# Optimization experiments

Hardware: AMD Instinct MI355X
Metric: run time of the kernel (lower is better)

The kernel has to match this reference:

```python
import jax, jax.numpy as jnp
import numpy as np

N = 100_000   # nodes
R = 8         # relations (edge types)
E = 100_000   # edges per relation
D_IN = 64
D_OUT = 64


def setup_inputs() -> dict:
    key = jax.random.key(0)
    k1, k2, k3, k4 = jax.random.split(key, 4)
    feat = jax.random.normal(k1, (N, D_IN), dtype=jnp.float32)
    # per-relation weight matrices (nn.ParameterDict in the original)
    weight = jax.random.normal(k2, (R, D_IN, D_OUT), dtype=jnp.float32) / np.sqrt(D_IN).astype(np.float32)
    edge_src = jax.random.randint(k3, (R, E), 0, N)
    edge_dst = jax.random.randint(k4, (R, E), 0, N)
    return {"feat": feat, "weight": weight, "edge_src": edge_src, "edge_dst": edge_dst}


def reference(feat, weight, edge_src, edge_dst):
    # Per-relation: gather src features, dense matmul with that relation's
    # weight, scatter-sum messages into destination nodes; 'sum' across
    # relations (cross-type reducer) collapses into one big scatter-add.
    n = feat.shape[0]
    gathered = feat[edge_src]                            # [R, E, d_in] irregular gather
    msg = jnp.einsum('red,rdf->ref', gathered, weight)   # [R, E, d_out]
    out = jax.ops.segment_sum(
        msg.reshape(-1, msg.shape[-1]),                  # [R*E, d_out]
        edge_dst.reshape(-1),
        num_segments=n,
    )                                                    # [N, d_out]
    return out
```

## Files before the change

### kernel.cpp

```cpp
#include <hip/hip_runtime.h>
#include <hip/hip_bf16.h>


#define WAVES_PER_BLOCK 4
#define EDGES_PER_WAVE 64
#define NGROUPS (EDGES_PER_WAVE / 4)
#define TILE_E (WAVES_PER_BLOCK * EDGES_PER_WAVE)

__global__ __launch_bounds__(256) void rgcn_edge_kernel(
    const float* __restrict__ feat,
    const float* __restrict__ weight,
    const int*   __restrict__ esrc,
    const int*   __restrict__ edst,
    float*       __restrict__ out,
    int E, int blocksPerRel)
{
    __shared__ float slab[WAVES_PER_BLOCK][4][64];

    const int t    = threadIdx.x;
    const int wave = t >> 6;
    const int lane = t & 63;

    const int r       = blockIdx.x / blocksPerRel;
    const int tileIdx = blockIdx.x % blocksPerRel;
    const int e0      = tileIdx * TILE_E + wave * EDGES_PER_WAVE;

    const float* wbase = weight + (size_t)r * 4096 + lane;
    float wreg[64];
    #pragma unroll
    for (int d = 0; d < 64; ++d) wreg[d] = wbase[(size_t)d * 64];

    const int sub = lane >> 4;
    const int q   = lane & 15;

    const int* srcR = esrc + (size_t)r * E;
    const int* dstR = edst + (size_t)r * E;

    auto load_group = [&](int gbase, float4& a, int dv[4]) {
        const int  e_g  = gbase + sub;
        const int  srow = (e_g < E) ? srcR[e_g] : 0;
        a = ((const float4*)(feat + (size_t)srow * 64))[q];
        if (gbase + 3 < E) {
            const int4 d4 = *(const int4*)(dstR + gbase);
            dv[0] = d4.x; dv[1] = d4.y; dv[2] = d4.z; dv[3] = d4.w;
        } else {
            #pragma unroll
            for (int s = 0; s < 4; ++s)
                dv[s] = (gbase + s < E) ? dstR[gbase + s] : 0;
        }
    };

    if (e0 >= E) return;

    float4 aCur; int dCur[4];
    load_group(e0, aCur, dCur);

    for (int g = 0; g < NGROUPS; ++g) {
        const int ebase = e0 + g * 4;
        if (ebase >= E) break;

        *(float4*)&slab[wave][sub][q * 4] = aCur;

        float4 aNxt = {0.f, 0.f, 0.f, 0.f};
        int dNxt[4] = {0, 0, 0, 0};
        const int enext = ebase + 4;
        const bool hasNext = (g + 1 < NGROUPS) && (enext < E);
        if (hasNext) load_group(enext, aNxt, dNxt);

        #pragma unroll
        for (int s = 0; s < 4; ++s) {
            const int e = ebase + s;
            if (e >= E) break;
            float acc = 0.f;
            #pragma unroll
            for (int d4 = 0; d4 < 16; ++d4) {
                const float4 av = *(const float4*)&slab[wave][s][d4 * 4];
                acc = fmaf(av.x, wreg[4 * d4 + 0], acc);
                acc = fmaf(av.y, wreg[4 * d4 + 1], acc);
                acc = fmaf(av.z, wreg[4 * d4 + 2], acc);
                acc = fmaf(av.w, wreg[4 * d4 + 3], acc);
            }
            atomicAdd(out + (size_t)dCur[s] * 64 + lane, acc);
        }

        aCur = aNxt;
        #pragma unroll
        for (int s = 0; s < 4; ++s) dCur[s] = dNxt[s];
    }
}

extern "C" void kernel_launch(void* const* d_in, const int* in_sizes, int n_in,
                              void* d_out, int out_size, void* d_ws, size_t ws_size,
                              hipStream_t stream) {
    const float* feat   = (const float*)d_in[0];
    const float* weight = (const float*)d_in[1];
    const int*   esrc   = (const int*)d_in[2];
    const int*   edst   = (const int*)d_in[3];
    float*       out    = (float*)d_out;

    const int R = in_sizes[1] / (64 * 64);
    const int E = in_sizes[2] / R;

    hipMemsetAsync(d_out, 0, (size_t)out_size * sizeof(float), stream);

    const int blocksPerRel = (E + TILE_E - 1) / TILE_E;
    const dim3 grid(R * blocksPerRel);
    const dim3 block(WAVES_PER_BLOCK * 64);
    rgcn_edge_kernel<<<grid, block, 0, stream>>>(feat, weight, esrc, edst, out,
                                                 E, blocksPerRel);
}
```

Baseline: 267.3 us.

## Broadcast edge indices via readlane and load source rows uniformly, dropping LDS staging

```diff
diff --git a/kernel.cpp b/kernel.cpp
--- a/kernel.cpp
+++ b/kernel.cpp
@@ -4,7 +4,6 @@
 
 #define WAVES_PER_BLOCK 4
 #define EDGES_PER_WAVE 64
-#define NGROUPS (EDGES_PER_WAVE / 4)
 #define TILE_E (WAVES_PER_BLOCK * EDGES_PER_WAVE)
 
 __global__ __launch_bounds__(256) void rgcn_edge_kernel(
@@ -15,8 +14,6 @@
     float*       __restrict__ out,
     int E, int blocksPerRel)
 {
-    __shared__ float slab[WAVES_PER_BLOCK][4][64];
-
     const int t    = threadIdx.x;
     const int wave = t >> 6;
     const int lane = t & 63;
@@ -24,68 +21,37 @@
     const int r       = blockIdx.x / blocksPerRel;
     const int tileIdx = blockIdx.x % blocksPerRel;
     const int e0      = tileIdx * TILE_E + wave * EDGES_PER_WAVE;
+    if (e0 >= E) return;
 
     const float* wbase = weight + (size_t)r * 4096 + lane;
     float wreg[64];
     #pragma unroll
     for (int d = 0; d < 64; ++d) wreg[d] = wbase[(size_t)d * 64];
 
-    const int sub = lane >> 4;
-    const int q   = lane & 15;
+    const int nE = min(EDGES_PER_WAVE, E - e0);
+    const int ei = e0 + min(lane, nE - 1);
+    const int sv = esrc[(size_t)r * E + ei];
+    const int dv = edst[(size_t)r * E + ei];
 
-    const int* srcR = esrc + (size_t)r * E;
-    const int* dstR = edst + (size_t)r * E;
+    float* outl = out + lane;
 
-    auto load_group = [&](int gbase, float4& a, int dv[4]) {
-        const int  e_g  = gbase + sub;
-        const int  srow = (e_g < E) ? srcR[e_g] : 0;
-        a = ((const float4*)(feat + (size_t)srow * 64))[q];
-        if (gbase + 3 < E) {
-            const int4 d4 = *(const int4*)(dstR + gbase);
-            dv[0] = d4.x; dv[1] = d4.y; dv[2] = d4.z; dv[3] = d4.w;
-        } else {
-            #pragma unroll
-            for (int s = 0; s < 4; ++s)
-                dv[s] = (gbase + s < E) ? dstR[gbase + s] : 0;
+    for (int i = 0; i < nE; ++i) {
+        const int srow = __builtin_amdgcn_readlane(sv, i);
+        const int drow = __builtin_amdgcn_readlane(dv, i);
+
+        const float4* xp = (const float4*)(feat + (size_t)srow * 64);
+        float a0 = 0.f, a1 = 0.f, a2 = 0.f, a3 = 0.f;
+        #pragma unroll
+        for (int c = 0; c < 16; ++c) {
+            const float4 v = xp[c];
+            a0 = fmaf(v.x, wreg[4 * c + 0], a0);
+            a1 = fmaf(v.y, wreg[4 * c + 1], a1);
+            a2 = fmaf(v.z, wreg[4 * c + 2], a2);
+            a3 = fmaf(v.w, wreg[4 * c + 3], a3);
         }
-    };
+        const float acc = (a0 + a1) + (a2 + a3);
 
-    if (e0 >= E) return;
-
-    float4 aCur; int dCur[4];
-    load_group(e0, aCur, dCur);
-
-    for (int g = 0; g < NGROUPS; ++g) {
-        const int ebase = e0 + g * 4;
-        if (ebase >= E) break;
-
-        *(float4*)&slab[wave][sub][q * 4] = aCur;
-
-        float4 aNxt = {0.f, 0.f, 0.f, 0.f};
-        int dNxt[4] = {0, 0, 0, 0};
-        const int enext = ebase + 4;
-        const bool hasNext = (g + 1 < NGROUPS) && (enext < E);
-        if (hasNext) load_group(enext, aNxt, dNxt);
-
-        #pragma unroll
-        for (int s = 0; s < 4; ++s) {
-            const int e = ebase + s;
-            if (e >= E) break;
-            float acc = 0.f;
-            #pragma unroll
-            for (int d4 = 0; d4 < 16; ++d4) {
-                const float4 av = *(const float4*)&slab[wave][s][d4 * 4];
-                acc = fmaf(av.x, wreg[4 * d4 + 0], acc);
-                acc = fmaf(av.y, wreg[4 * d4 + 1], acc);
-                acc = fmaf(av.z, wreg[4 * d4 + 2], acc);
-                acc = fmaf(av.w, wreg[4 * d4 + 3], acc);
-            }
-            atomicAdd(out + (size_t)dCur[s] * 64 + lane, acc);
-        }
-
-        aCur = aNxt;
-        #pragma unroll
-        for (int s = 0; s < 4; ++s) dCur[s] = dNxt[s];
+        atomicAdd(outl + (size_t)drow * 64, acc);
     }
 }
 
```

After: 263.9 us. Within noise of the previous version (-1.3%).
